# Kernel optimization log

Hardware: AMD Instinct MI355X
Metric: run time of the kernel (lower is better)

Reference implementation:

```python
import jax, jax.numpy as jnp
import numpy as np

NUM_HEADS = 16

def setup_inputs() -> dict:
    key = jax.random.key(0)
    ks = jax.random.split(key, 7)
    b, sq, sk, d = 2, 2048, 2048, 1024
    return {
        "query": jax.random.normal(ks[0], (b, sq, d), dtype=jnp.float32),
        "key": jax.random.normal(ks[1], (b, sk, d), dtype=jnp.float32),
        "value": jax.random.normal(ks[2], (b, sk, d), dtype=jnp.float32),
        "key_mask": jax.random.randint(ks[3], (b, sk, 1), 0, 2, dtype=jnp.int32),
        "query_mask": jax.random.randint(ks[4], (b, sq, 1), 0, 2, dtype=jnp.int32),
        "Wo": jax.random.normal(ks[5], (d, d), dtype=jnp.float32) * 0.02,
        "bo": jnp.zeros((d,), dtype=jnp.float32),
    }

def reference(query, key, value, key_mask, query_mask, Wo, bo):
    b, s_q, d = query.shape
    s_k = key.shape[1]
    h = NUM_HEADS
    hd = d // h
    q = query.reshape(b, s_q, h, hd).transpose(0, 2, 1, 3)   # [b,h,sq,hd]
    k = key.reshape(b, s_k, h, hd).transpose(0, 2, 1, 3)     # [b,h,sk,hd]
    v = value.reshape(b, s_k, h, hd).transpose(0, 2, 1, 3)   # [b,h,sk,hd]
    scores = jnp.einsum('bhqd,bhkd->bhqk', q, k) / jnp.sqrt(jnp.float32(hd))
    # dual masking: key_mask [b,sk,1] -> [b,1,1,sk]; query_mask [b,sq,1] -> [b,1,sq,1]
    km = (key_mask[:, :, 0] != 0)[:, None, None, :]
    qm = (query_mask[:, :, 0] != 0)[:, None, :, None]
    valid = km & qm                                           # [b,1,sq,sk]
    scores = jnp.where(valid, scores, -jnp.inf)
    # safe softmax: fully-masked rows -> softmax over zeros, then zeroed out
    # (matches torch: softmax over all -inf gives NaN, nan_to_num -> 0.0)
    row_valid = jnp.any(valid, axis=-1, keepdims=True)        # [b,1,sq,1]
    safe_scores = jnp.where(row_valid, scores, 0.0)
    w = jax.nn.softmax(safe_scores, axis=-1)
    w = jnp.where(row_valid, w, 0.0)
    # dropout is identity (eval mode / p=0)
    out = jnp.einsum('bhqk,bhkd->bhqd', w, v)                 # [b,h,sq,hd]
    out = out.transpose(0, 2, 1, 3).reshape(b, s_q, d)
    return out @ Wo.T + bo
```

## Files before the change

### kernel.cpp

```cpp
#include <hip/hip_runtime.h>

typedef __bf16 bfv8 __attribute__((ext_vector_type(8)));
typedef float f32x4 __attribute__((ext_vector_type(4)));
typedef short s16x8 __attribute__((ext_vector_type(8)));
typedef unsigned int u32;
typedef unsigned int u32x4 __attribute__((ext_vector_type(4)));

#define MFMA16(a,b,c) __builtin_amdgcn_mfma_f32_16x16x32_bf16((a),(b),(c),0,0,0)

__device__ __forceinline__ u32 pk2(float a, float b){
  u32 r; asm("v_cvt_pk_bf16_f32 %0, %1, %2" : "=v"(r) : "v"(a), "v"(b)); return r;
}
__device__ __forceinline__ bfv8 cvt8s(const float* p, float s){
  u32x4 r;
  #pragma unroll
  for (int j=0;j<4;++j) r[j] = pk2(p[2*j]*s, p[2*j+1]*s);
  return *(bfv8*)&r;
}
__device__ __forceinline__ void glds16(const short* g, short* l){
  __builtin_amdgcn_global_load_lds(
      (const __attribute__((address_space(1))) u32*)g,
      (__attribute__((address_space(3))) u32*)l, 16, 0, 0);
}
__device__ __forceinline__ void glds16f(const float* g, float* l){
  __builtin_amdgcn_global_load_lds(
      (const __attribute__((address_space(1))) u32*)g,
      (__attribute__((address_space(3))) u32*)l, 16, 0, 0);
}

__global__ __launch_bounds__(256) void prep(const float* __restrict__ K, const float* __restrict__ V,
                                            const float* __restrict__ Wo, const int* __restrict__ km,
                                            short* __restrict__ Kt, short* __restrict__ Vt,
                                            short* __restrict__ Wb, float* __restrict__ kb){
  __shared__ short tl[64][65];
  const int bid = blockIdx.x, tid = threadIdx.x;
  if (bid < 2048){
    int idx = bid*256 + tid;
    int cs = idx & 7, r = (idx >> 3) & 63, kt = (idx >> 9) & 31, bh = idx >> 14;
    int b = bh >> 4, h = bh & 15;
    int c = cs ^ (r & 7);
    const float* src = K + ((size_t)(b*2048 + kt*64 + r))*1024 + h*64 + c*8;
    float4 a = ((const float4*)src)[0], bb = ((const float4*)src)[1];
    u32x4 o;
    o[0]=pk2(a.x,a.y); o[1]=pk2(a.z,a.w); o[2]=pk2(bb.x,bb.y); o[3]=pk2(bb.z,bb.w);
    ((u32x4*)Kt)[idx] = o;
  } else if (bid < 3072){
    int vb = bid - 2048;
    int kt = vb & 31, bh = vb >> 5;
    int b = bh >> 4, h = bh & 15;
    {
      int s = tid >> 2, d0 = (tid & 3) * 16;
      const float* src = V + ((size_t)(b*2048 + kt*64 + s))*1024 + h*64 + d0;
      #pragma unroll
      for (int j = 0; j < 4; ++j){
        float4 v = ((const float4*)src)[j];
        tl[d0+4*j+0][s] = (short)(pk2(v.x, v.x) & 0xffff);
        tl[d0+4*j+1][s] = (short)(pk2(v.y, v.y) & 0xffff);
        tl[d0+4*j+2][s] = (short)(pk2(v.z, v.z) & 0xffff);
        tl[d0+4*j+3][s] = (short)(pk2(v.w, v.w) & 0xffff);
      }
    }
    __syncthreads();
    {
      int r = tid >> 2, cp = (tid & 3) * 2;
      short* dst = Vt + (((size_t)(bh*32 + kt)*64 + r) << 6);
      #pragma unroll
      for (int q = 0; q < 2; ++q){
        int cs = cp + q;
        int c = cs ^ (r & 7);
        s16x8 o;
        #pragma unroll
        for (int j = 0; j < 8; ++j){
          int s = c*8 + j;
          int sg = s >> 2, rr = s & 3;
          int t = (sg >> 3)*2 + (sg & 1);
          int a = (sg >> 1) & 3;
          int kap = t*16 + a*4 + rr;
          o[j] = tl[r][kap];
        }
        *(s16x8*)(dst + cs*8) = o;
      }
    }
  } else if (bid < 3584){
    int i = (bid - 3072)*256 + tid;
    const float* p = Wo + (size_t)i*8;
    u32x4 o;
    o[0]=pk2(p[0],p[1]); o[1]=pk2(p[2],p[3]); o[2]=pk2(p[4],p[5]); o[3]=pk2(p[6],p[7]);
    ((u32x4*)Wb)[i] = o;
  } else {
    int i = (bid - 3584)*256 + tid;
    if (i < 4096) kb[i] = (km[i] != 0) ? 0.0f : -1e30f;
  }
}

__global__ __launch_bounds__(512, 4) void attn7(const short* __restrict__ Kt, const short* __restrict__ Vt,
                                                const float* __restrict__ Qf, const float* __restrict__ kbias,
                                                const int* __restrict__ qmask, short* __restrict__ X){
  __shared__ __align__(16) short kl[4][64][64];
  __shared__ __align__(16) short vl[4][64][64];
  __shared__ __align__(16) float blds[2048];
  const int wid = blockIdx.x;
  const int bh = (wid & 7)*4 + (wid >> 7);
  const int qt = (wid >> 3) & 15;
  const int b = bh >> 4, h = bh & 15;
  const int tid = threadIdx.x;
  const int w = tid >> 6, lane = tid & 63, lo = lane & 15, hi = lane >> 4;

  const float QSCALE = 0.125f * 1.44269504088896f;
  const int qrow = qt*128 + w*16 + lo;
  bfv8 qf0, qf1;
  {
    const float* qp = Qf + ((size_t)(b*2048 + qrow))*1024 + h*64 + hi*8;
    qf0 = cvt8s(qp, QSCALE);
    qf1 = cvt8s(qp + 32, QSCALE);
  }
  const short* ktb = Kt + ((size_t)(bh*32) << 12);
  const short* vtb = Vt + ((size_t)(bh*32) << 12);
  const float* kbb = kbias + b*2048;

  const int sgoff = w*512 + lane*8;
  const int csK   = (hi ^ (lo & 7)) * 8;

  f32x4 acc[4];
  #pragma unroll
  for (int t2=0;t2<4;++t2) acc[t2] = (f32x4){0.f,0.f,0.f,0.f};
  f32x4 accL = (f32x4){0.f,0.f,0.f,0.f};
  const u32x4 onesw = (u32x4){0x3F803F80u,0x3F803F80u,0x3F803F80u,0x3F803F80u};
  const bfv8 ones = *(const bfv8*)&onesw;

  glds16f(kbb + w*256 + lane*4, blds + w*256);
  #pragma unroll
  for (int p = 0; p < 3; ++p){
    glds16(ktb + ((size_t)p << 12) + sgoff, &kl[p][0][0] + w*512);
    glds16(vtb + ((size_t)p << 12) + sgoff, &vl[p][0][0] + w*512);
  }

  for (int kt = 0; kt < 32; ++kt){
    asm volatile("s_waitcnt vmcnt(4)" ::: "memory");
    __builtin_amdgcn_s_barrier();
    {
      const int tn = (kt + 3) & 31, bn = (kt + 3) & 3;
      glds16(ktb + ((size_t)tn << 12) + sgoff, &kl[bn][0][0] + w*512);
      glds16(vtb + ((size_t)tn << 12) + sgoff, &vl[bn][0][0] + w*512);
    }
    const short (*kc)[64] = kl[kt & 3];
    const short (*vc)[64] = vl[kt & 3];
    const int k0 = kt*64;

    u32 pk[8];
    __builtin_amdgcn_s_setprio(1);
    #pragma unroll
    for (int t=0;t<4;++t){
      f32x4 bv = *(const f32x4*)&blds[k0 + t*16 + 4*hi];
      const short* rowp = &kc[t*16+lo][0];
      bfv8 kf0 = *(const bfv8*)(rowp + csK);
      bfv8 kf1 = *(const bfv8*)(rowp + (csK ^ 32));
      f32x4 c = MFMA16(kf0, qf0, bv);
      c = MFMA16(kf1, qf1, c);
      float p0 = __builtin_amdgcn_exp2f(c[0]);
      float p1 = __builtin_amdgcn_exp2f(c[1]);
      float p2 = __builtin_amdgcn_exp2f(c[2]);
      float p3 = __builtin_amdgcn_exp2f(c[3]);
      pk[2*t]   = pk2(p0, p1);
      pk[2*t+1] = pk2(p2, p3);
    }
    __builtin_amdgcn_s_setprio(0);
    u32x4 pw0 = {pk[0],pk[1],pk[2],pk[3]};
    u32x4 pw1 = {pk[4],pk[5],pk[6],pk[7]};
    bfv8 pb0 = *(bfv8*)&pw0, pb1 = *(bfv8*)&pw1;

    __builtin_amdgcn_s_setprio(1);
    accL = MFMA16(ones, pb0, accL);
    accL = MFMA16(ones, pb1, accL);
    #pragma unroll
    for (int t2=0;t2<4;++t2){
      const short* rowp = &vc[t2*16+lo][0];
      bfv8 vf0 = *(const bfv8*)(rowp + csK);
      bfv8 vf1 = *(const bfv8*)(rowp + (csK ^ 32));
      acc[t2] = MFMA16(vf0, pb0, acc[t2]);
      acc[t2] = MFMA16(vf1, pb1, acc[t2]);
    }
    __builtin_amdgcn_s_setprio(0);
  }
  asm volatile("s_waitcnt vmcnt(0)" ::: "memory");

  float l = accL[0];
  float inv = (l > 0.f) ? 1.0f/l : 0.f;
  if (qmask[b*2048 + qrow] == 0) inv = 0.f;
  u32* xp = (u32*)(X + ((size_t)(b*2048 + qrow))*1024 + h*64);
  #pragma unroll
  for (int t2=0;t2<4;++t2){
    xp[t2*8 + 2*hi]     = pk2(acc[t2][0]*inv, acc[t2][1]*inv);
    xp[t2*8 + 2*hi + 1] = pk2(acc[t2][2]*inv, acc[t2][3]*inv);
  }
}

__global__ __launch_bounds__(256) void proj2(const short* __restrict__ X, const short* __restrict__ Wb,
                                             const float* __restrict__ bo, float* __restrict__ Y){
  __shared__ __align__(16) short xl[4][128][32];
  __shared__ __align__(16) short wl[4][64][32];
  const int bid = blockIdx.x;
  const int xcd = bid & 7, ii = bid >> 3;
  const int by = xcd*4 + (ii >> 4);
  const int bx = ii & 15;
  const int tid = threadIdx.x;
  const int w = tid >> 6, lane = tid & 63, lo = lane & 15, hi = lane >> 4;
  const int wr = w >> 1, wc = w & 1;
  const int brow = by*128, bcol = bx*64;

  const int cx0 = (w*2+0)*64 + lane, cx1 = (w*2+1)*64 + lane, cw0 = w*64 + lane;
  const int rx0 = cx0 >> 2, rx1 = cx1 >> 2, rw0 = cw0 >> 2;
  const short* xs0 = X  + (size_t)(brow + rx0)*1024 + ((cx0 & 3) ^ (rx0 & 3))*8;
  const short* xs1 = X  + (size_t)(brow + rx1)*1024 + ((cx1 & 3) ^ (rx1 & 3))*8;
  const short* ws0 = Wb + (size_t)(bcol + rw0)*1024 + ((cw0 & 3) ^ (rw0 & 3))*8;

  const int csA = (hi ^ (lo & 3)) * 8;

  f32x4 acc[4][2];
  #pragma unroll
  for (int i=0;i<4;++i){ acc[i][0] = (f32x4){0.f,0.f,0.f,0.f}; acc[i][1] = (f32x4){0.f,0.f,0.f,0.f}; }

  #pragma unroll
  for (int p = 0; p < 3; ++p){
    glds16(xs0 + p*32, &xl[p][0][0] + (w*2+0)*512);
    glds16(xs1 + p*32, &xl[p][0][0] + (w*2+1)*512);
    glds16(ws0 + p*32, &wl[p][0][0] + w*512);
  }

  for (int kt = 0; kt < 32; ++kt){
    asm volatile("s_waitcnt vmcnt(6)" ::: "memory");
    __builtin_amdgcn_s_barrier();
    {
      const int tn = (kt + 3) & 31, bn = (kt + 3) & 3;
      glds16(xs0 + tn*32, &xl[bn][0][0] + (w*2+0)*512);
      glds16(xs1 + tn*32, &xl[bn][0][0] + (w*2+1)*512);
      glds16(ws0 + tn*32, &wl[bn][0][0] + w*512);
    }
    const short* xc = &xl[kt & 3][0][0];
    const short* wcp = &wl[kt & 3][0][0];
    bfv8 a[4], bb[2];
    #pragma unroll
    for (int i=0;i<4;++i) a[i]  = *(const bfv8*)(xc  + (wr*64 + i*16 + lo)*32 + csA);
    #pragma unroll
    for (int j=0;j<2;++j) bb[j] = *(const bfv8*)(wcp + (wc*32 + j*16 + lo)*32 + csA);
    __builtin_amdgcn_s_setprio(1);
    #pragma unroll
    for (int i=0;i<4;++i){
      acc[i][0] = MFMA16(a[i], bb[0], acc[i][0]);
      acc[i][1] = MFMA16(a[i], bb[1], acc[i][1]);
    }
    __builtin_amdgcn_s_setprio(0);
  }
  asm volatile("s_waitcnt vmcnt(0)" ::: "memory");

  float bv[2];
  bv[0] = bo[bcol + wc*32 + lo];
  bv[1] = bo[bcol + wc*32 + 16 + lo];
  #pragma unroll
  for (int i=0;i<4;++i){
    #pragma unroll
    for (int r=0;r<4;++r){
      size_t row = (size_t)(brow + wr*64 + i*16 + hi*4 + r);
      float* yp = Y + row*1024 + bcol + wc*32 + lo;
      yp[0]  = acc[i][0][r] + bv[0];
      yp[16] = acc[i][1][r] + bv[1];
    }
  }
}

extern "C" void kernel_launch(void* const* d_in, const int* in_sizes, int n_in,
                              void* d_out, int out_size, void* d_ws, size_t ws_size,
                              hipStream_t stream){
  const float* Q   = (const float*)d_in[0];
  const float* K   = (const float*)d_in[1];
  const float* V   = (const float*)d_in[2];
  const int* key_mask   = (const int*)d_in[3];
  const int* query_mask = (const int*)d_in[4];
  const float* Wo  = (const float*)d_in[5];
  const float* bo  = (const float*)d_in[6];

  short* Ktw = (short*)d_ws;
  short* Vtw = Ktw + 4194304;
  short* Wb  = Vtw + 4194304;
  short* Xb  = Wb + 1048576;
  float* kbf = (float*)(Xb + 4194304);

  prep<<<3600,256,0,stream>>>(K, V, Wo, key_mask, Ktw, Vtw, Wb, kbf);
  attn7<<<512,512,0,stream>>>(Ktw, Vtw, Q, kbf, query_mask, Xb);
  proj2<<<512,256,0,stream>>>(Xb, Wb, bo, (float*)d_out);
}
```

Baseline: 78.11 us.

## Fold key mask into V and row-sum instead of additive score bias

The key mask is now applied by zeroing masked rows of V during prep. The softmax denominator uses a permuted bf16 mask vector in the row-sum MFMA in place of an all-ones operand, so the per-tile float bias load from LDS and the biased MFMA accumulator init are gone. Each block also starts its key-tile loop at a rotated offset to spread L2/HBM traffic, and sched_barrier and compiler fences are added around the async LDS loads. Because no max subtraction is done, exp2 of unmasked scores is computed over all keys, with overflow risk as before. Masked keys now contribute nothing instead of underflowing to zero.

```diff
diff --git a/kernel.cpp b/kernel.cpp
--- a/kernel.cpp
+++ b/kernel.cpp
@@ -22,16 +22,11 @@
       (const __attribute__((address_space(1))) u32*)g,
       (__attribute__((address_space(3))) u32*)l, 16, 0, 0);
 }
-__device__ __forceinline__ void glds16f(const float* g, float* l){
-  __builtin_amdgcn_global_load_lds(
-      (const __attribute__((address_space(1))) u32*)g,
-      (__attribute__((address_space(3))) u32*)l, 16, 0, 0);
-}
 
 __global__ __launch_bounds__(256) void prep(const float* __restrict__ K, const float* __restrict__ V,
                                             const float* __restrict__ Wo, const int* __restrict__ km,
                                             short* __restrict__ Kt, short* __restrict__ Vt,
-                                            short* __restrict__ Wb, float* __restrict__ kb){
+                                            short* __restrict__ Wb, short* __restrict__ kms){
   __shared__ short tl[64][65];
   const int bid = blockIdx.x, tid = threadIdx.x;
   if (bid < 2048){
@@ -50,14 +45,15 @@
     int b = bh >> 4, h = bh & 15;
     {
       int s = tid >> 2, d0 = (tid & 3) * 16;
+      float kmv = (km[b*2048 + kt*64 + s] != 0) ? 1.0f : 0.0f;
       const float* src = V + ((size_t)(b*2048 + kt*64 + s))*1024 + h*64 + d0;
       #pragma unroll
       for (int j = 0; j < 4; ++j){
         float4 v = ((const float4*)src)[j];
-        tl[d0+4*j+0][s] = (short)(pk2(v.x, v.x) & 0xffff);
-        tl[d0+4*j+1][s] = (short)(pk2(v.y, v.y) & 0xffff);
-        tl[d0+4*j+2][s] = (short)(pk2(v.z, v.z) & 0xffff);
-        tl[d0+4*j+3][s] = (short)(pk2(v.w, v.w) & 0xffff);
+        tl[d0+4*j+0][s] = (short)(pk2(v.x*kmv, 0.f) & 0xffff);
+        tl[d0+4*j+1][s] = (short)(pk2(v.y*kmv, 0.f) & 0xffff);
+        tl[d0+4*j+2][s] = (short)(pk2(v.z*kmv, 0.f) & 0xffff);
+        tl[d0+4*j+3][s] = (short)(pk2(v.w*kmv, 0.f) & 0xffff);
       }
     }
     __syncthreads();
@@ -89,23 +85,30 @@
     ((u32x4*)Wb)[i] = o;
   } else {
     int i = (bid - 3584)*256 + tid;
-    if (i < 4096) kb[i] = (km[i] != 0) ? 0.0f : -1e30f;
-  }
-}
-
-__global__ __launch_bounds__(512, 4) void attn7(const short* __restrict__ Kt, const short* __restrict__ Vt,
-                                                const float* __restrict__ Qf, const float* __restrict__ kbias,
+    if (i < 4096){
+      int bb = i >> 11, kt = (i >> 6) & 31, s = i & 63;
+      int rr = s & 3, a = (s >> 3) & 3, t = ((s >> 5) & 1)*2 + ((s >> 2) & 1);
+      int key = t*16 + a*4 + rr;
+      kms[i] = (km[bb*2048 + kt*64 + key] != 0) ? (short)0x3F80 : (short)0;
+    }
+  }
+}
+
+__global__ __launch_bounds__(512, 4) void attn8(const short* __restrict__ Kt, const short* __restrict__ Vt,
+                                                const float* __restrict__ Qf, const short* __restrict__ kms,
                                                 const int* __restrict__ qmask, short* __restrict__ X){
   __shared__ __align__(16) short kl[4][64][64];
   __shared__ __align__(16) short vl[4][64][64];
-  __shared__ __align__(16) float blds[2048];
+  __shared__ __align__(16) short kml[32][64];
   const int wid = blockIdx.x;
   const int bh = (wid & 7)*4 + (wid >> 7);
   const int qt = (wid >> 3) & 15;
   const int b = bh >> 4, h = bh & 15;
   const int tid = threadIdx.x;
   const int w = tid >> 6, lane = tid & 63, lo = lane & 15, hi = lane >> 4;
-
+  const int toff = (wid * 7) & 31;
+
+  const f32x4 ZERO4 = {0.f, 0.f, 0.f, 0.f};
   const float QSCALE = 0.125f * 1.44269504088896f;
   const int qrow = qt*128 + w*16 + lo;
   bfv8 qf0, qf1;
@@ -114,48 +117,58 @@
     qf0 = cvt8s(qp, QSCALE);
     qf1 = cvt8s(qp + 32, QSCALE);
   }
+
+  if (w < 4) glds16(kms + b*2048 + w*512 + lane*8, &kml[0][0] + w*512);
+  asm volatile("s_waitcnt vmcnt(0)" ::: "memory");
+  __builtin_amdgcn_s_barrier();
+  __builtin_amdgcn_sched_barrier(0);
+
   const short* ktb = Kt + ((size_t)(bh*32) << 12);
   const short* vtb = Vt + ((size_t)(bh*32) << 12);
-  const float* kbb = kbias + b*2048;
 
   const int sgoff = w*512 + lane*8;
   const int csK   = (hi ^ (lo & 7)) * 8;
 
   f32x4 acc[4];
   #pragma unroll
-  for (int t2=0;t2<4;++t2) acc[t2] = (f32x4){0.f,0.f,0.f,0.f};
-  f32x4 accL = (f32x4){0.f,0.f,0.f,0.f};
-  const u32x4 onesw = (u32x4){0x3F803F80u,0x3F803F80u,0x3F803F80u,0x3F803F80u};
-  const bfv8 ones = *(const bfv8*)&onesw;
-
-  glds16f(kbb + w*256 + lane*4, blds + w*256);
+  for (int t2=0;t2<4;++t2) acc[t2] = ZERO4;
+  f32x4 accL = ZERO4;
+
   #pragma unroll
   for (int p = 0; p < 3; ++p){
-    glds16(ktb + ((size_t)p << 12) + sgoff, &kl[p][0][0] + w*512);
-    glds16(vtb + ((size_t)p << 12) + sgoff, &vl[p][0][0] + w*512);
-  }
-
-  for (int kt = 0; kt < 32; ++kt){
+    const int tp = (toff + p) & 31;
+    glds16(ktb + ((size_t)tp << 12) + sgoff, &kl[p][0][0] + w*512);
+    asm volatile("" ::: "memory");
+    glds16(vtb + ((size_t)tp << 12) + sgoff, &vl[p][0][0] + w*512);
+    asm volatile("" ::: "memory");
+  }
+
+  for (int i = 0; i < 32; ++i){
     asm volatile("s_waitcnt vmcnt(4)" ::: "memory");
     __builtin_amdgcn_s_barrier();
+    __builtin_amdgcn_sched_barrier(0);
     {
-      const int tn = (kt + 3) & 31, bn = (kt + 3) & 3;
+      const int tn = (toff + i + 3) & 31, bn = (i + 3) & 3;
       glds16(ktb + ((size_t)tn << 12) + sgoff, &kl[bn][0][0] + w*512);
+      asm volatile("" ::: "memory");
       glds16(vtb + ((size_t)tn << 12) + sgoff, &vl[bn][0][0] + w*512);
-    }
-    const short (*kc)[64] = kl[kt & 3];
-    const short (*vc)[64] = vl[kt & 3];
-    const int k0 = kt*64;
+      asm volatile("" ::: "memory");
+    }
+    const short (*kc)[64] = kl[i & 3];
+    const short (*vc)[64] = vl[i & 3];
+    const int tcur = (toff + i) & 31;
+    const short* kmrow = &kml[tcur][0];
+    bfv8 kmf0 = *(const bfv8*)(kmrow + hi*8);
+    bfv8 kmf1 = *(const bfv8*)(kmrow + 32 + hi*8);
 
     u32 pk[8];
     __builtin_amdgcn_s_setprio(1);
     #pragma unroll
     for (int t=0;t<4;++t){
-      f32x4 bv = *(const f32x4*)&blds[k0 + t*16 + 4*hi];
       const short* rowp = &kc[t*16+lo][0];
       bfv8 kf0 = *(const bfv8*)(rowp + csK);
       bfv8 kf1 = *(const bfv8*)(rowp + (csK ^ 32));
-      f32x4 c = MFMA16(kf0, qf0, bv);
+      f32x4 c = MFMA16(kf0, qf0, ZERO4);
       c = MFMA16(kf1, qf1, c);
       float p0 = __builtin_amdgcn_exp2f(c[0]);
       float p1 = __builtin_amdgcn_exp2f(c[1]);
@@ -170,8 +183,8 @@
     bfv8 pb0 = *(bfv8*)&pw0, pb1 = *(bfv8*)&pw1;
 
     __builtin_amdgcn_s_setprio(1);
-    accL = MFMA16(ones, pb0, accL);
-    accL = MFMA16(ones, pb1, accL);
+    accL = MFMA16(kmf0, pb0, accL);
+    accL = MFMA16(kmf1, pb1, accL);
     #pragma unroll
     for (int t2=0;t2<4;++t2){
       const short* rowp = &vc[t2*16+lo][0];
@@ -207,6 +220,7 @@
   const int w = tid >> 6, lane = tid & 63, lo = lane & 15, hi = lane >> 4;
   const int wr = w >> 1, wc = w & 1;
   const int brow = by*128, bcol = bx*64;
+  const f32x4 ZERO4 = {0.f, 0.f, 0.f, 0.f};
 
   const int cx0 = (w*2+0)*64 + lane, cx1 = (w*2+1)*64 + lane, cw0 = w*64 + lane;
   const int rx0 = cx0 >> 2, rx1 = cx1 >> 2, rw0 = cw0 >> 2;
@@ -218,23 +232,30 @@
 
   f32x4 acc[4][2];
   #pragma unroll
-  for (int i=0;i<4;++i){ acc[i][0] = (f32x4){0.f,0.f,0.f,0.f}; acc[i][1] = (f32x4){0.f,0.f,0.f,0.f}; }
+  for (int i=0;i<4;++i){ acc[i][0] = ZERO4; acc[i][1] = ZERO4; }
 
   #pragma unroll
   for (int p = 0; p < 3; ++p){
     glds16(xs0 + p*32, &xl[p][0][0] + (w*2+0)*512);
+    asm volatile("" ::: "memory");
     glds16(xs1 + p*32, &xl[p][0][0] + (w*2+1)*512);
+    asm volatile("" ::: "memory");
     glds16(ws0 + p*32, &wl[p][0][0] + w*512);
+    asm volatile("" ::: "memory");
   }
 
   for (int kt = 0; kt < 32; ++kt){
     asm volatile("s_waitcnt vmcnt(6)" ::: "memory");
     __builtin_amdgcn_s_barrier();
+    __builtin_amdgcn_sched_barrier(0);
     {
       const int tn = (kt + 3) & 31, bn = (kt + 3) & 3;
       glds16(xs0 + tn*32, &xl[bn][0][0] + (w*2+0)*512);
+      asm volatile("" ::: "memory");
       glds16(xs1 + tn*32, &xl[bn][0][0] + (w*2+1)*512);
+      asm volatile("" ::: "memory");
       glds16(ws0 + tn*32, &wl[bn][0][0] + w*512);
+      asm volatile("" ::: "memory");
     }
     const short* xc = &xl[kt & 3][0][0];
     const short* wcp = &wl[kt & 3][0][0];
@@ -283,9 +304,9 @@
   short* Vtw = Ktw + 4194304;
   short* Wb  = Vtw + 4194304;
   short* Xb  = Wb + 1048576;
-  float* kbf = (float*)(Xb + 4194304);
-
-  prep<<<3600,256,0,stream>>>(K, V, Wo, key_mask, Ktw, Vtw, Wb, kbf);
-  attn7<<<512,512,0,stream>>>(Ktw, Vtw, Q, kbf, query_mask, Xb);
+  short* kms = Xb + 4194304;
+
+  prep<<<3600,256,0,stream>>>(K, V, Wo, key_mask, Ktw, Vtw, Wb, kms);
+  attn8<<<512,512,0,stream>>>(Ktw, Vtw, Q, kms, query_mask, Xb);
   proj2<<<512,256,0,stream>>>(Xb, Wb, bo, (float*)d_out);
 }
```

Measured after the change: 78.31 us. Within noise of the previous version (+0.2%).
